# Optimization experiments

Hardware: AMD Instinct MI355X
Metric: run time of the kernel (lower is better)

The kernel has to match this reference:

```python
import jax, jax.numpy as jnp
import numpy as np

B, S, F, D = 2, 576, 16, 512   # batch, spatial tokens (24x24), frames, query_dim
H, C = 8, 64                   # heads, dim_head; inner = H*C = 512


def setup_inputs() -> dict:
    key = jax.random.key(0)
    ks = jax.random.split(key, 6)
    x = jax.random.normal(ks[0], (B, S, F, D), jnp.float32)
    # alternating drop pattern over frames 2..F-1; identical per batch row,
    # as the module requires (it reshapes kept indices to [bs, -1] and takes
    # valid_num from row 0)
    pat = jnp.tile(jnp.array([1, 0], jnp.int64), (F - 2) // 2)
    drop_mask = jnp.broadcast_to(pat, (B, F - 2))
    sd = 1.0 / np.sqrt(D)
    Wq = jax.random.normal(ks[1], (D, H * C), jnp.float32) * sd
    Wk = jax.random.normal(ks[2], (D, H * C), jnp.float32) * sd
    Wv = jax.random.normal(ks[3], (D, H * C), jnp.float32) * sd
    Wout = jax.random.normal(ks[4], (H * C, D), jnp.float32) * (1.0 / np.sqrt(H * C))
    bout = jnp.zeros((D,), jnp.float32)
    return {"x": x, "drop_mask": drop_mask, "Wq": Wq, "Wk": Wk, "Wv": Wv,
            "Wout": Wout, "bout": bout}


def _sdpa(q, k, v):
    # q: [..., Lq, C], k/v: [..., Lk, C]; xformers default scale = 1/sqrt(C)
    scale = 1.0 / np.sqrt(q.shape[-1])
    logits = jnp.einsum('...qc,...kc->...qk', q, k) * scale
    w = jax.nn.softmax(logits, axis=-1)
    return jnp.einsum('...qk,...kc->...qc', w, v)


def reference(x, drop_mask, Wq, Wk, Wv, Wout, bout):
    b, s, f, _ = x.shape
    h, c = H, C
    q = x @ Wq  # [b, s, f, h*c]
    k = x @ Wk
    v = x @ Wv

    # ---- per-frame spatial self-attention for frames 1: ('b s f (h c) -> (b f h) s c')
    def to_bfhsc(t, nf):
        return t.reshape(b, s, nf, h, c).transpose(0, 2, 3, 1, 4)  # b f h s c

    ress = _sdpa(to_bfhsc(q[:, :, 1:], f - 1),
                 to_bfhsc(k[:, :, 1:], f - 1),
                 to_bfhsc(v[:, :, 1:], f - 1))            # [b, f-1, h, s, c]
    ress = ress.transpose(0, 3, 1, 2, 4).reshape(b, s, f - 1, h * c)

    # ---- frame-0 temporal attention over first 2 frames + non-dropped frames
    dm = np.asarray(drop_mask)
    valid = int((f - 2) - dm[0].sum())
    # kept frame indices (into frames 2..f-1), per batch row
    kept = np.stack([np.nonzero(dm[i] == 0)[0] for i in range(b)])  # [b, valid]
    idx = jnp.asarray(kept)[:, None, :, None]
    ka, va = k[:, :, 2:], v[:, :, 2:]                     # [b, s, f-2, h*c]
    ki = jnp.take_along_axis(ka, jnp.broadcast_to(idx, (b, s, valid, h * c)), axis=2)
    vi = jnp.take_along_axis(va, jnp.broadcast_to(idx, (b, s, valid, h * c)), axis=2)
    dk = jnp.concatenate([k[:, :, :2], ki], axis=2)        # [b, s, df, h*c]
    dv = jnp.concatenate([v[:, :, :2], vi], axis=2)
    df = 2 + valid

    qt = q[:, :, 0].reshape(b, s, h, c).transpose(0, 2, 1, 3)  # [b, h, s, c]
    kt = dk.reshape(b, s, df, h, c).transpose(0, 3, 1, 2, 4).reshape(b, h, s * df, c)
    vt = dv.reshape(b, s, df, h, c).transpose(0, 3, 1, 2, 4).reshape(b, h, s * df, c)
    resq = _sdpa(qt, kt, vt)                               # [b, h, s, c]
    resq = resq.transpose(0, 2, 1, 3).reshape(b, s, 1, h * c)

    res = jnp.concatenate([resq, ress], axis=2)            # [b, s, f, h*c]
    return res @ Wout + bout                               # [b, s, f, D]
```

## Files before the change

kernel.cpp:

```cpp
#include <hip/hip_runtime.h>
#include <math.h>

#define Bb 2
#define Ss 576
#define Ff 16
#define Hh 8
#define Cc 64
#define HC 512
#define Mrows (Bb * Ss * Ff)

typedef __bf16 bf16x8 __attribute__((ext_vector_type(8)));
typedef float  f32x4  __attribute__((ext_vector_type(4)));
typedef float  f32x16 __attribute__((ext_vector_type(16)));
typedef unsigned short u16;
typedef unsigned int   u32;

#if __has_builtin(__builtin_amdgcn_exp2f)
#define EXP2(x) __builtin_amdgcn_exp2f(x)
#else
#define EXP2(x) exp2f(x)
#endif

#define QSCALE 0.18033688011112042f

__device__ __forceinline__ u16 f2bf(float f) {
    union { __bf16 b; u16 u; } cv;
    cv.b = (__bf16)f;
    return cv.u;
}

__device__ __forceinline__ f32x16 zero16() {
    f32x16 z;
#pragma unroll
    for (int i = 0; i < 16; ++i) z[i] = 0.f;
    return z;
}

__device__ __forceinline__ int swz8(int row, int g) {
    return row * 64 + (((g ^ (row & 7) ^ (((row >> 3) & 1) << 1)) & 7) << 3);
}

__device__ __forceinline__ uint4 pack8(float4 a, float4 b) {
    union { u16 s[8]; uint4 v; } u;
    u.s[0] = f2bf(a.x); u.s[1] = f2bf(a.y); u.s[2] = f2bf(a.z); u.s[3] = f2bf(a.w);
    u.s[4] = f2bf(b.x); u.s[5] = f2bf(b.y); u.s[6] = f2bf(b.z); u.s[7] = f2bf(b.w);
    return u.v;
}

__device__ __forceinline__ void gl_lds16(const u16* g, u16* l) {
    __builtin_amdgcn_global_load_lds(
        (const __attribute__((address_space(1))) u32*)g,
        (__attribute__((address_space(3))) u32*)l, 16, 0, 0);
}

__global__ __launch_bounds__(256) void convert_x_kernel(
    const float* __restrict__ x, u16* __restrict__ xb)
{
    size_t i = ((size_t)blockIdx.x * 256 + threadIdx.x) * 8;
    float4 a = *(const float4*)&x[i];
    float4 b = *(const float4*)&x[i + 4];
    *(uint4*)&xb[i] = pack8(a, b);
}

__global__ __launch_bounds__(256) void convert_w_kernel(
    const float* __restrict__ W0, const float* __restrict__ W1,
    const float* __restrict__ W2, const float* __restrict__ W3,
    u16* __restrict__ Wt)
{
    __shared__ float Ts[64][65];
    const int mz = blockIdx.z;
    const float* W = (mz == 0) ? W0 : (mz == 1) ? W1 : (mz == 2) ? W2 : W3;
    u16* Wo = Wt + (size_t)mz * 512 * 512;
    const int k0 = blockIdx.x * 64, n0 = blockIdx.y * 64;
    const int t = threadIdx.x;
#pragma unroll
    for (int p = 0; p < 4; ++p) {
        int idx = t + p * 256;
        int row = idx >> 4, cg = idx & 15;
        *(float4*)&Ts[row][cg * 4] =
            *(const float4*)&W[(size_t)(k0 + row) * 512 + n0 + cg * 4];
    }
    __syncthreads();
#pragma unroll
    for (int p = 0; p < 2; ++p) {
        int idx = t + p * 256;
        int row = idx >> 3, cg = idx & 7;
        union { u16 s[8]; uint4 v; } u;
#pragma unroll
        for (int j = 0; j < 8; ++j) u.s[j] = f2bf(Ts[cg * 8 + j][row]);
        *(uint4*)&Wo[(size_t)(n0 + row) * 512 + k0 + cg * 8] = u.v;
    }
}

__global__ __launch_bounds__(256) void qkv_kernel(
    const u16* __restrict__ xb, const u16* __restrict__ Wt,
    u16* __restrict__ q, u16* __restrict__ k, u16* __restrict__ vT)
{
    __shared__ u16 As[128 * 32];
    __shared__ u16 Bs[128 * 32];
    const int bi = blockIdx.x;
    const int mt = bi % 144;
    const int mm = bi / 144;
    const int nt = mm & 3, mat = mm >> 2;
    const int t = threadIdx.x;
    const int w = t >> 6, L = t & 63;
    const int m0 = mt * 128, n0 = nt * 128;
    const int wm = (w >> 1) * 64, wn = (w & 1) * 64;

    const int srow = t >> 2, scg = t & 3;
    const int ma0 = m0 + srow, ma1 = ma0 + 64;
    const int b0 = ma0 / 9216, r0 = ma0 % 9216, f0 = r0 / 576, s0 = r0 % 576;
    const int b1 = ma1 / 9216, r1 = ma1 % 9216, f1 = r1 / 576, s1 = r1 % 576;
    const u16* xp0 = xb + ((size_t)(b0 * 576 + s0) * 16 + f0) * 512 + scg * 8;
    const u16* xp1 = xb + ((size_t)(b1 * 576 + s1) * 16 + f1) * 512 + scg * 8;
    const u16* Bp = Wt + (size_t)mat * 512 * 512 + (size_t)(n0 + srow) * 512 + scg * 8;

    f32x4 acc[4][4];
#pragma unroll
    for (int i = 0; i < 4; ++i)
#pragma unroll
        for (int j = 0; j < 4; ++j) acc[i][j] = (f32x4){0.f, 0.f, 0.f, 0.f};

    for (int k0 = 0; k0 < 512; k0 += 32) {
        __syncthreads();
        gl_lds16(xp0 + k0, &As[t * 8]);
        gl_lds16(xp1 + k0, &As[2048 + t * 8]);
        gl_lds16(Bp + k0, &Bs[t * 8]);
        gl_lds16(Bp + k0 + 64 * 512, &Bs[2048 + t * 8]);
        __syncthreads();
        bf16x8 af[4], bfr[4];
#pragma unroll
        for (int i = 0; i < 4; ++i) {
            af[i]  = *(const bf16x8*)&As[(wm + 16 * i + (L & 15)) * 32 + (L >> 4) * 8];
            bfr[i] = *(const bf16x8*)&Bs[(wn + 16 * i + (L & 15)) * 32 + (L >> 4) * 8];
        }
#pragma unroll
        for (int i = 0; i < 4; ++i)
#pragma unroll
            for (int j = 0; j < 4; ++j)
                acc[i][j] = __builtin_amdgcn_mfma_f32_16x16x32_bf16(
                    af[i], bfr[j], acc[i][j], 0, 0, 0);
    }

    if (mat < 2) {
        u16* Cout = (mat == 0) ? q : k;
        const float scale = (mat == 0) ? QSCALE : 1.0f;
#pragma unroll
        for (int i = 0; i < 4; ++i)
#pragma unroll
            for (int j = 0; j < 4; ++j)
#pragma unroll
                for (int r = 0; r < 4; ++r) {
                    int row = m0 + wm + 16 * i + (L >> 4) * 4 + r;
                    int col = n0 + wn + 16 * j + (L & 15);
                    float vv = acc[i][j][r] * scale;
                    float pvv = __shfl_xor(vv, 1);
                    if (!(L & 1)) {
                        u32 pk2 = (u32)f2bf(vv) | ((u32)f2bf(pvv) << 16);
                        *(u32*)(Cout + (size_t)row * 512 + col) = pk2;
                    }
                }
    } else {
#pragma unroll
        for (int i = 0; i < 4; ++i) {
            int row = m0 + wm + 16 * i + (L >> 4) * 4;
            int bb = row / 9216, rr = row % 9216;
            int f = rr / 576, s = rr % 576;
#pragma unroll
            for (int j = 0; j < 4; ++j) {
                int col = n0 + wn + 16 * j + (L & 15);
                int h = col >> 6, c = col & 63;
                union { u16 s4[4]; uint2 v; } u;
#pragma unroll
                for (int r = 0; r < 4; ++r) u.s4[r] = f2bf(acc[i][j][r]);
                *(uint2*)&vT[((((size_t)(bb * 16 + f) * 8 + h) * 64 + c) * 576) + s] = u.v;
            }
        }
    }
}

__global__ __launch_bounds__(256) void gemm_out_kernel(
    const u16* __restrict__ res, const u16* __restrict__ Wt3,
    const float* __restrict__ bout, float* __restrict__ out)
{
    __shared__ u16 As[128 * 32];
    __shared__ u16 Bs[128 * 32];
    const int bi = blockIdx.x;
    const int mt = bi % 144, nt = bi / 144;
    const int t = threadIdx.x;
    const int w = t >> 6, L = t & 63;
    const int m0 = mt * 128, n0 = nt * 128;
    const int wm = (w >> 1) * 64, wn = (w & 1) * 64;

    const int srow = t >> 2, scg = t & 3;
    const u16* Ap = res + (size_t)(m0 + srow) * 512 + scg * 8;
    const u16* Bp = Wt3 + (size_t)(n0 + srow) * 512 + scg * 8;

    f32x4 acc[4][4];
#pragma unroll
    for (int i = 0; i < 4; ++i)
#pragma unroll
        for (int j = 0; j < 4; ++j) acc[i][j] = (f32x4){0.f, 0.f, 0.f, 0.f};

    for (int k0 = 0; k0 < 512; k0 += 32) {
        __syncthreads();
        gl_lds16(Ap + k0, &As[t * 8]);
        gl_lds16(Ap + k0 + 64 * 512, &As[2048 + t * 8]);
        gl_lds16(Bp + k0, &Bs[t * 8]);
        gl_lds16(Bp + k0 + 64 * 512, &Bs[2048 + t * 8]);
        __syncthreads();
        bf16x8 af[4], bfr[4];
#pragma unroll
        for (int i = 0; i < 4; ++i) {
            af[i]  = *(const bf16x8*)&As[(wm + 16 * i + (L & 15)) * 32 + (L >> 4) * 8];
            bfr[i] = *(const bf16x8*)&Bs[(wn + 16 * i + (L & 15)) * 32 + (L >> 4) * 8];
        }
#pragma unroll
        for (int i = 0; i < 4; ++i)
#pragma unroll
            for (int j = 0; j < 4; ++j)
                acc[i][j] = __builtin_amdgcn_mfma_f32_16x16x32_bf16(
                    af[i], bfr[j], acc[i][j], 0, 0, 0);
    }

#pragma unroll
    for (int i = 0; i < 4; ++i)
#pragma unroll
        for (int r = 0; r < 4; ++r) {
            int row = m0 + wm + 16 * i + (L >> 4) * 4 + r;
            int bb = row / 9216, rr = row % 9216;
            int f = rr / 576, s = rr % 576;
            size_t obase = ((size_t)(bb * 576 + s) * 16 + f) * 512;
#pragma unroll
            for (int j = 0; j < 4; ++j) {
                int col = n0 + wn + 16 * j + (L & 15);
                out[obase + col] = acc[i][j][r] + bout[col];
            }
        }
}

__global__ __launch_bounds__(256, 4) void attn_kernel(
    const u16* __restrict__ q, const u16* __restrict__ k,
    const u16* __restrict__ vT, const int* __restrict__ dm,
    u16* __restrict__ res, float* __restrict__ po, float* __restrict__ pl)
{
    __shared__ u16 Ks[64 * 64];
    __shared__ u16 Vts[64 * 64];

    const int t = threadIdx.x;
    const int w = t >> 6, L = t & 63;
    const int half = L >> 5, l31 = L & 31;
    const int bi = blockIdx.x;

    int b, h, qt, qframe, fi, mode;
    if (bi < 720) {
        mode = 0;
        qt = bi / 144;
        int g = bi % 144;
        int bh = g / 9; fi = g % 9;
        b = bh >> 3; h = bh & 7; qframe = 0;
    } else {
        mode = 1;
        int u = bi - 720;
        int g = u % 240;
        qt = u / 240;
        b = g / 120;
        int rr = g % 120;
        qframe = 1 + (rr >> 3); h = rr & 7; fi = 0;
    }

    int kf;
    if (mode == 1) {
        kf = qframe;
    } else if (fi < 2) {
        kf = fi;
    } else {
        int n = 2; kf = 2;
#pragma unroll
        for (int j = 0; j < Ff - 2; ++j) {
            if (dm[b * (Ff - 2) + j] == 0) { if (n == fi) kf = 2 + j; ++n; }
        }
    }

    const int q0 = qt * 128;
    const bool active = (q0 + 32 * w) < Ss;
    const int qrow = q0 + 32 * w + l31;

    bf16x8 qf[4];
    if (active) {
        const u16* qp = q + ((size_t)(b * 16 + qframe) * Ss + qrow) * 512 + h * 64 + 8 * half;
#pragma unroll
        for (int ks = 0; ks < 4; ++ks) qf[ks] = *(const bf16x8*)(qp + 16 * ks);
    }

    float lsum = 0.f;
    f32x16 o[2] = {zero16(), zero16()};

    const int srow = t >> 2, sc2 = (t & 3) * 2;
    const int lk0 = swz8(srow, sc2), lk1 = swz8(srow, sc2 + 1);
    const u16* kbase = k + ((size_t)(b * 16 + kf) * Ss) * 512 + h * 64;
    const u16* vbase = vT + (((size_t)(b * 16 + kf) * 8 + h) * 64) * (size_t)Ss;

    uint4 ka, kb2, va, vb2;
    {
        const u16* kp = kbase + (size_t)srow * 512 + sc2 * 8;
        ka  = *(const uint4*)kp;
        kb2 = *(const uint4*)(kp + 8);
        const u16* vp = vbase + (size_t)srow * Ss + sc2 * 8;
        va  = *(const uint4*)vp;
        vb2 = *(const uint4*)(vp + 8);
    }

    for (int kt = 0; kt < 9; ++kt) {
        __syncthreads();
        *(uint4*)&Ks[lk0]  = ka;
        *(uint4*)&Ks[lk1]  = kb2;
        *(uint4*)&Vts[lk0] = va;
        *(uint4*)&Vts[lk1] = vb2;
        __syncthreads();

        if (kt < 8) {
            int s0 = (kt + 1) * 64;
            const u16* kp = kbase + (size_t)(s0 + srow) * 512 + sc2 * 8;
            ka  = *(const uint4*)kp;
            kb2 = *(const uint4*)(kp + 8);
            const u16* vp = vbase + (size_t)srow * Ss + s0 + sc2 * 8;
            va  = *(const uint4*)vp;
            vb2 = *(const uint4*)(vp + 8);
        }

        if (active) {
#pragma unroll
            for (int hb = 0; hb < 2; ++hb) {
                f32x16 st = zero16();
#pragma unroll
                for (int ks = 0; ks < 4; ++ks) {
                    bf16x8 a = *(const bf16x8*)&Ks[swz8(32 * hb + l31, 2 * ks + half)];
                    st = __builtin_amdgcn_mfma_f32_32x32x16_bf16(a, qf[ks], st, 0, 0, 0);
                }
#pragma unroll
                for (int kk = 0; kk < 2; ++kk) {
                    const int ks = 2 * hb + kk;
                    float e0 = EXP2(st[8 * kk + 0]), e1 = EXP2(st[8 * kk + 1]);
                    float e2 = EXP2(st[8 * kk + 2]), e3 = EXP2(st[8 * kk + 3]);
                    float e4 = EXP2(st[8 * kk + 4]), e5 = EXP2(st[8 * kk + 5]);
                    float e6 = EXP2(st[8 * kk + 6]), e7 = EXP2(st[8 * kk + 7]);
                    lsum += ((e0 + e1) + (e2 + e3)) + ((e4 + e5) + (e6 + e7));
                    u32 x0 = (u32)f2bf(e0) | ((u32)f2bf(e1) << 16);
                    u32 z0 = (u32)f2bf(e2) | ((u32)f2bf(e3) << 16);
                    u32 x1 = (u32)f2bf(e4) | ((u32)f2bf(e5) << 16);
                    u32 z1 = (u32)f2bf(e6) | ((u32)f2bf(e7) << 16);
                    auto sx = __builtin_amdgcn_permlane32_swap(x0, x1, false, false);
                    auto sz = __builtin_amdgcn_permlane32_swap(z0, z1, false, false);
                    union { u32 u[4]; bf16x8 v; } pu;
                    pu.u[0] = sx[0]; pu.u[1] = sz[0]; pu.u[2] = sx[1]; pu.u[3] = sz[1];
                    bf16x8 v0 = *(const bf16x8*)&Vts[swz8(l31,      2 * ks + half)];
                    bf16x8 v1 = *(const bf16x8*)&Vts[swz8(32 + l31, 2 * ks + half)];
                    o[0] = __builtin_amdgcn_mfma_f32_32x32x16_bf16(v0, pu.v, o[0], 0, 0, 0);
                    o[1] = __builtin_amdgcn_mfma_f32_32x32x16_bf16(v1, pu.v, o[1], 0, 0, 0);
                }
            }
        }
    }

    if (!active) return;
    lsum += __shfl_xor(lsum, 32);

    if (mode == 1) {
        float inv = 1.f / lsum;
        u16* rp = res + ((size_t)(b * 16 + qframe) * Ss + qrow) * 512 + h * 64;
#pragma unroll
        for (int cg = 0; cg < 2; ++cg)
#pragma unroll
            for (int g = 0; g < 4; ++g) {
                union { u16 s4[4]; uint2 v; } u;
#pragma unroll
                for (int r = 0; r < 4; ++r) u.s4[r] = f2bf(o[cg][4 * g + r] * inv);
                *(uint2*)&rp[32 * cg + 8 * g + 4 * half] = u.v;
            }
    } else {
        int bh = b * 8 + h;
        float* pp = po + ((size_t)(fi * 16 + bh) * Ss + qrow) * 64;
#pragma unroll
        for (int cg = 0; cg < 2; ++cg)
#pragma unroll
            for (int g = 0; g < 4; ++g) {
                float4 v4 = make_float4(o[cg][4 * g + 0], o[cg][4 * g + 1],
                                        o[cg][4 * g + 2], o[cg][4 * g + 3]);
                *(float4*)&pp[32 * cg + 8 * g + 4 * half] = v4;
            }
        if (half == 0) pl[(size_t)(fi * 16 + bh) * Ss + qrow] = lsum;
    }
}

__global__ __launch_bounds__(256) void merge_kernel(
    const float* __restrict__ po, const float* __restrict__ pl,
    u16* __restrict__ res)
{
    int tid = blockIdx.x * 256 + threadIdx.x;
    int c4 = tid & 15;
    int rem = tid >> 4;
    int qg = rem % Ss;
    int bh = rem / Ss;
    int b = bh >> 3, h = bh & 7;
    float4 acc = make_float4(0.f, 0.f, 0.f, 0.f);
    float ls = 0.f;
#pragma unroll
    for (int fi = 0; fi < 9; ++fi) {
        const float4 v = *(const float4*)&po[((size_t)(fi * 16 + bh) * Ss + qg) * 64 + c4 * 4];
        acc.x += v.x; acc.y += v.y; acc.z += v.z; acc.w += v.w;
        ls += pl[(size_t)(fi * 16 + bh) * Ss + qg];
    }
    float inv = 1.f / ls;
    union { u16 s4[4]; uint2 v; } u;
    u.s4[0] = f2bf(acc.x * inv); u.s4[1] = f2bf(acc.y * inv);
    u.s4[2] = f2bf(acc.z * inv); u.s4[3] = f2bf(acc.w * inv);
    *(uint2*)&res[((size_t)(b * 16 + 0) * Ss + qg) * 512 + h * 64 + c4 * 4] = u.v;
}

extern "C" void kernel_launch(void* const* d_in, const int* in_sizes, int n_in,
                              void* d_out, int out_size, void* d_ws, size_t ws_size,
                              hipStream_t stream)
{
    (void)in_sizes; (void)n_in; (void)out_size; (void)ws_size;
    const float* x    = (const float*)d_in[0];
    const int*   dmsk = (const int*)  d_in[1];
    const float* Wq   = (const float*)d_in[2];
    const float* Wk   = (const float*)d_in[3];
    const float* Wv   = (const float*)d_in[4];
    const float* Wout = (const float*)d_in[5];
    const float* bout = (const float*)d_in[6];
    float* out = (float*)d_out;

    const size_t NE = (size_t)Mrows * HC;
    u16* q   = (u16*)d_ws;
    u16* kk  = q   + NE;
    u16* vT  = kk  + NE;
    u16* res = vT  + NE;
    u16* Wt  = res + NE;
    float* po = (float*)(Wt + (size_t)4 * 512 * 512);
    float* pl = po + (size_t)9 * 16 * Ss * 64;
    u16* xb = res;

    convert_x_kernel<<<4608, 256, 0, stream>>>(x, xb);
    convert_w_kernel<<<dim3(8, 8, 4), 256, 0, stream>>>(Wq, Wk, Wv, Wout, Wt);
    qkv_kernel<<<1728, 256, 0, stream>>>(xb, Wt, q, kk, vT);
    attn_kernel<<<1920, 256, 0, stream>>>(q, kk, vT, dmsk, res, po, pl);
    merge_kernel<<<576, 256, 0, stream>>>(po, pl, res);
    gemm_out_kernel<<<576, 256, 0, stream>>>(
        res, Wt + (size_t)3 * 512 * 512, bout, out);
}
```

Before: 228.5 us.

## Double-buffer LDS tiles in GEMM and attention kernels; merge convert kernels

Converts the QKV GEMM, output GEMM and attention K/V loops from single-buffered LDS with two barriers per step to ping-pong double buffering with one barrier per step. The next tile's global-to-LDS loads are issued before the current tile's MFMAs so that memory latency overlaps with compute. It also fuses the x and weight conversion kernels into one launch, saving a kernel launch. The cost is double the shared memory per block, which may lower occupancy.

```diff
diff --git a/kernel.cpp b/kernel.cpp
--- a/kernel.cpp
+++ b/kernel.cpp
@@ -53,26 +53,26 @@
         (__attribute__((address_space(3))) u32*)l, 16, 0, 0);
 }
 
-__global__ __launch_bounds__(256) void convert_x_kernel(
-    const float* __restrict__ x, u16* __restrict__ xb)
-{
-    size_t i = ((size_t)blockIdx.x * 256 + threadIdx.x) * 8;
-    float4 a = *(const float4*)&x[i];
-    float4 b = *(const float4*)&x[i + 4];
-    *(uint4*)&xb[i] = pack8(a, b);
-}
-
-__global__ __launch_bounds__(256) void convert_w_kernel(
+__global__ __launch_bounds__(256) void prep_kernel(
     const float* __restrict__ W0, const float* __restrict__ W1,
     const float* __restrict__ W2, const float* __restrict__ W3,
-    u16* __restrict__ Wt)
+    const float* __restrict__ x,
+    u16* __restrict__ Wt, u16* __restrict__ xb)
 {
     __shared__ float Ts[64][65];
     const int mz = blockIdx.z;
+    const int t = threadIdx.x;
+    if (mz >= 4) {
+        int id = (mz - 4) * 64 + blockIdx.y * 8 + blockIdx.x;
+        size_t i = ((size_t)id * 256 + t) * 8;
+        float4 a = *(const float4*)&x[i];
+        float4 b = *(const float4*)&x[i + 4];
+        *(uint4*)&xb[i] = pack8(a, b);
+        return;
+    }
     const float* W = (mz == 0) ? W0 : (mz == 1) ? W1 : (mz == 2) ? W2 : W3;
     u16* Wo = Wt + (size_t)mz * 512 * 512;
     const int k0 = blockIdx.x * 64, n0 = blockIdx.y * 64;
-    const int t = threadIdx.x;
 #pragma unroll
     for (int p = 0; p < 4; ++p) {
         int idx = t + p * 256;
@@ -96,8 +96,8 @@
     const u16* __restrict__ xb, const u16* __restrict__ Wt,
     u16* __restrict__ q, u16* __restrict__ k, u16* __restrict__ vT)
 {
-    __shared__ u16 As[128 * 32];
-    __shared__ u16 Bs[128 * 32];
+    __shared__ u16 As[2 * 128 * 32];
+    __shared__ u16 Bs[2 * 128 * 32];
     const int bi = blockIdx.x;
     const int mt = bi % 144;
     const int mm = bi / 144;
@@ -106,6 +106,7 @@
     const int w = t >> 6, L = t & 63;
     const int m0 = mt * 128, n0 = nt * 128;
     const int wm = (w >> 1) * 64, wn = (w & 1) * 64;
+    const int t8 = t * 8;
 
     const int srow = t >> 2, scg = t & 3;
     const int ma0 = m0 + srow, ma1 = ma0 + 64;
@@ -121,18 +122,30 @@
 #pragma unroll
         for (int j = 0; j < 4; ++j) acc[i][j] = (f32x4){0.f, 0.f, 0.f, 0.f};
 
-    for (int k0 = 0; k0 < 512; k0 += 32) {
-        __syncthreads();
-        gl_lds16(xp0 + k0, &As[t * 8]);
-        gl_lds16(xp1 + k0, &As[2048 + t * 8]);
-        gl_lds16(Bp + k0, &Bs[t * 8]);
-        gl_lds16(Bp + k0 + 64 * 512, &Bs[2048 + t * 8]);
-        __syncthreads();
+    gl_lds16(xp0, &As[t8]);
+    gl_lds16(xp1, &As[2048 + t8]);
+    gl_lds16(Bp,  &Bs[t8]);
+    gl_lds16(Bp + 64 * 512, &Bs[2048 + t8]);
+    __syncthreads();
+
+    int cur = 0;
+    for (int t16 = 0; t16 < 16; ++t16) {
+        if (t16 < 15) {
+            const int kn = (t16 + 1) * 32;
+            u16* An = As + (cur ^ 1) * 4096;
+            u16* Bn = Bs + (cur ^ 1) * 4096;
+            gl_lds16(xp0 + kn, &An[t8]);
+            gl_lds16(xp1 + kn, &An[2048 + t8]);
+            gl_lds16(Bp + kn,  &Bn[t8]);
+            gl_lds16(Bp + kn + 64 * 512, &Bn[2048 + t8]);
+        }
+        const u16* Ac = As + cur * 4096;
+        const u16* Bc = Bs + cur * 4096;
         bf16x8 af[4], bfr[4];
 #pragma unroll
         for (int i = 0; i < 4; ++i) {
-            af[i]  = *(const bf16x8*)&As[(wm + 16 * i + (L & 15)) * 32 + (L >> 4) * 8];
-            bfr[i] = *(const bf16x8*)&Bs[(wn + 16 * i + (L & 15)) * 32 + (L >> 4) * 8];
+            af[i]  = *(const bf16x8*)&Ac[(wm + 16 * i + (L & 15)) * 32 + (L >> 4) * 8];
+            bfr[i] = *(const bf16x8*)&Bc[(wn + 16 * i + (L & 15)) * 32 + (L >> 4) * 8];
         }
 #pragma unroll
         for (int i = 0; i < 4; ++i)
@@ -140,6 +153,8 @@
             for (int j = 0; j < 4; ++j)
                 acc[i][j] = __builtin_amdgcn_mfma_f32_16x16x32_bf16(
                     af[i], bfr[j], acc[i][j], 0, 0, 0);
+        __syncthreads();
+        cur ^= 1;
     }
 
     if (mat < 2) {
@@ -183,14 +198,15 @@
     const u16* __restrict__ res, const u16* __restrict__ Wt3,
     const float* __restrict__ bout, float* __restrict__ out)
 {
-    __shared__ u16 As[128 * 32];
-    __shared__ u16 Bs[128 * 32];
+    __shared__ u16 As[2 * 128 * 32];
+    __shared__ u16 Bs[2 * 128 * 32];
     const int bi = blockIdx.x;
     const int mt = bi % 144, nt = bi / 144;
     const int t = threadIdx.x;
     const int w = t >> 6, L = t & 63;
     const int m0 = mt * 128, n0 = nt * 128;
     const int wm = (w >> 1) * 64, wn = (w & 1) * 64;
+    const int t8 = t * 8;
 
     const int srow = t >> 2, scg = t & 3;
     const u16* Ap = res + (size_t)(m0 + srow) * 512 + scg * 8;
@@ -202,18 +218,30 @@
 #pragma unroll
         for (int j = 0; j < 4; ++j) acc[i][j] = (f32x4){0.f, 0.f, 0.f, 0.f};
 
-    for (int k0 = 0; k0 < 512; k0 += 32) {
-        __syncthreads();
-        gl_lds16(Ap + k0, &As[t * 8]);
-        gl_lds16(Ap + k0 + 64 * 512, &As[2048 + t * 8]);
-        gl_lds16(Bp + k0, &Bs[t * 8]);
-        gl_lds16(Bp + k0 + 64 * 512, &Bs[2048 + t * 8]);
-        __syncthreads();
+    gl_lds16(Ap, &As[t8]);
+    gl_lds16(Ap + 64 * 512, &As[2048 + t8]);
+    gl_lds16(Bp, &Bs[t8]);
+    gl_lds16(Bp + 64 * 512, &Bs[2048 + t8]);
+    __syncthreads();
+
+    int cur = 0;
+    for (int t16 = 0; t16 < 16; ++t16) {
+        if (t16 < 15) {
+            const int kn = (t16 + 1) * 32;
+            u16* An = As + (cur ^ 1) * 4096;
+            u16* Bn = Bs + (cur ^ 1) * 4096;
+            gl_lds16(Ap + kn, &An[t8]);
+            gl_lds16(Ap + kn + 64 * 512, &An[2048 + t8]);
+            gl_lds16(Bp + kn, &Bn[t8]);
+            gl_lds16(Bp + kn + 64 * 512, &Bn[2048 + t8]);
+        }
+        const u16* Ac = As + cur * 4096;
+        const u16* Bc = Bs + cur * 4096;
         bf16x8 af[4], bfr[4];
 #pragma unroll
         for (int i = 0; i < 4; ++i) {
-            af[i]  = *(const bf16x8*)&As[(wm + 16 * i + (L & 15)) * 32 + (L >> 4) * 8];
-            bfr[i] = *(const bf16x8*)&Bs[(wn + 16 * i + (L & 15)) * 32 + (L >> 4) * 8];
+            af[i]  = *(const bf16x8*)&Ac[(wm + 16 * i + (L & 15)) * 32 + (L >> 4) * 8];
+            bfr[i] = *(const bf16x8*)&Bc[(wn + 16 * i + (L & 15)) * 32 + (L >> 4) * 8];
         }
 #pragma unroll
         for (int i = 0; i < 4; ++i)
@@ -221,6 +249,8 @@
             for (int j = 0; j < 4; ++j)
                 acc[i][j] = __builtin_amdgcn_mfma_f32_16x16x32_bf16(
                     af[i], bfr[j], acc[i][j], 0, 0, 0);
+        __syncthreads();
+        cur ^= 1;
     }
 
 #pragma unroll
@@ -244,8 +274,8 @@
     const u16* __restrict__ vT, const int* __restrict__ dm,
     u16* __restrict__ res, float* __restrict__ po, float* __restrict__ pl)
 {
-    __shared__ u16 Ks[64 * 64];
-    __shared__ u16 Vts[64 * 64];
+    __shared__ u16 Ks[2 * 64 * 64];
+    __shared__ u16 Vts[2 * 64 * 64];
 
     const int t = threadIdx.x;
     const int w = t >> 6, L = t & 63;
@@ -310,17 +340,32 @@
         va  = *(const uint4*)vp;
         vb2 = *(const uint4*)(vp + 8);
     }
-
+    *(uint4*)&Ks[lk0]  = ka;
+    *(uint4*)&Ks[lk1]  = kb2;
+    *(uint4*)&Vts[lk0] = va;
+    *(uint4*)&Vts[lk1] = vb2;
+    {
+        const u16* kp = kbase + (size_t)(64 + srow) * 512 + sc2 * 8;
+        ka  = *(const uint4*)kp;
+        kb2 = *(const uint4*)(kp + 8);
+        const u16* vp = vbase + (size_t)srow * Ss + 64 + sc2 * 8;
+        va  = *(const uint4*)vp;
+        vb2 = *(const uint4*)(vp + 8);
+    }
+    __syncthreads();
+
+    int cur = 0;
     for (int kt = 0; kt < 9; ++kt) {
-        __syncthreads();
-        *(uint4*)&Ks[lk0]  = ka;
-        *(uint4*)&Ks[lk1]  = kb2;
-        *(uint4*)&Vts[lk0] = va;
-        *(uint4*)&Vts[lk1] = vb2;
-        __syncthreads();
-
         if (kt < 8) {
-            int s0 = (kt + 1) * 64;
+            u16* Kn = Ks + (cur ^ 1) * 4096;
+            u16* Vn = Vts + (cur ^ 1) * 4096;
+            *(uint4*)&Kn[lk0] = ka;
+            *(uint4*)&Kn[lk1] = kb2;
+            *(uint4*)&Vn[lk0] = va;
+            *(uint4*)&Vn[lk1] = vb2;
+        }
+        if (kt < 7) {
+            int s0 = (kt + 2) * 64;
             const u16* kp = kbase + (size_t)(s0 + srow) * 512 + sc2 * 8;
             ka  = *(const uint4*)kp;
             kb2 = *(const uint4*)(kp + 8);
@@ -330,12 +375,14 @@
         }
 
         if (active) {
+            const u16* Kc = Ks + cur * 4096;
+            const u16* Vc = Vts + cur * 4096;
 #pragma unroll
             for (int hb = 0; hb < 2; ++hb) {
                 f32x16 st = zero16();
 #pragma unroll
                 for (int ks = 0; ks < 4; ++ks) {
-                    bf16x8 a = *(const bf16x8*)&Ks[swz8(32 * hb + l31, 2 * ks + half)];
+                    bf16x8 a = *(const bf16x8*)&Kc[swz8(32 * hb + l31, 2 * ks + half)];
                     st = __builtin_amdgcn_mfma_f32_32x32x16_bf16(a, qf[ks], st, 0, 0, 0);
                 }
 #pragma unroll
@@ -354,13 +401,15 @@
                     auto sz = __builtin_amdgcn_permlane32_swap(z0, z1, false, false);
                     union { u32 u[4]; bf16x8 v; } pu;
                     pu.u[0] = sx[0]; pu.u[1] = sz[0]; pu.u[2] = sx[1]; pu.u[3] = sz[1];
-                    bf16x8 v0 = *(const bf16x8*)&Vts[swz8(l31,      2 * ks + half)];
-                    bf16x8 v1 = *(const bf16x8*)&Vts[swz8(32 + l31, 2 * ks + half)];
+                    bf16x8 v0 = *(const bf16x8*)&Vc[swz8(l31,      2 * ks + half)];
+                    bf16x8 v1 = *(const bf16x8*)&Vc[swz8(32 + l31, 2 * ks + half)];
                     o[0] = __builtin_amdgcn_mfma_f32_32x32x16_bf16(v0, pu.v, o[0], 0, 0, 0);
                     o[1] = __builtin_amdgcn_mfma_f32_32x32x16_bf16(v1, pu.v, o[1], 0, 0, 0);
                 }
             }
         }
+        __syncthreads();
+        cur ^= 1;
     }
 
     if (!active) return;
@@ -442,8 +491,7 @@
     float* pl = po + (size_t)9 * 16 * Ss * 64;
     u16* xb = res;
 
-    convert_x_kernel<<<4608, 256, 0, stream>>>(x, xb);
-    convert_w_kernel<<<dim3(8, 8, 4), 256, 0, stream>>>(Wq, Wk, Wv, Wout, Wt);
+    prep_kernel<<<dim3(8, 8, 76), 256, 0, stream>>>(Wq, Wk, Wv, Wout, x, Wt, xb);
     qkv_kernel<<<1728, 256, 0, stream>>>(xb, Wt, q, kk, vT);
     attn_kernel<<<1920, 256, 0, stream>>>(q, kk, vT, dmsk, res, po, pl);
     merge_kernel<<<576, 256, 0, stream>>>(po, pl, res);
```

Measured after the change: 287.5 us. 1.26x slower.
